# Performance work log

Hardware: AMD Instinct MI355X
Metric: run time of the kernel (lower is better)

## Reference

```python
import jax, jax.numpy as jnp
import numpy as np

DIM = 768
NUM_HEADS = 12
HEAD_DIM = DIM // NUM_HEADS
SCALE = HEAD_DIM ** (-0.5)
WH, WW = 14, 14
NUM_EXTRA = 1
NUM_REL_DIST = (2 * WH - 1) * (2 * WW - 1) + NUM_EXTRA * (NUM_EXTRA + 2)  # 732
N_TOK = WH * WW + NUM_EXTRA  # 197
BATCH = 64


def make_rel_pos_index():
    # mirrors the torch buffer construction (meshgrid 'ij')
    coords = np.stack(np.meshgrid(np.arange(WH), np.arange(WW), indexing='ij'))  # [2,Wh,Ww]
    coords_flat = coords.reshape(2, -1)  # [2, Wh*Ww]
    rel = coords_flat[:, :, None] - coords_flat[:, None, :]  # [2, M, M]
    rel = rel.transpose(1, 2, 0).astype(np.int64)  # [M, M, 2]
    rel[:, :, 0] += WH - 1
    rel[:, :, 1] += WW - 1
    rel[:, :, 0] *= 2 * WW - 1
    idx = np.zeros((N_TOK, N_TOK), dtype=np.int64)
    idx[NUM_EXTRA:, NUM_EXTRA:] = rel.sum(-1)
    idx[0, 0:] = NUM_REL_DIST - 3
    idx[0:, 0] = NUM_REL_DIST - 2
    idx[0, 0] = NUM_REL_DIST - 1
    return jnp.asarray(idx, dtype=jnp.int32)


def setup_inputs() -> dict:
    key = jax.random.key(0)
    ks = jax.random.split(key, 7)
    x = jax.random.normal(ks[0], (BATCH, N_TOK, DIM), dtype=jnp.float32)
    qkv_w = jax.random.normal(ks[1], (3 * DIM, DIM), dtype=jnp.float32) * (DIM ** -0.5)
    q_bias = jax.random.normal(ks[2], (DIM,), dtype=jnp.float32) * 0.02
    v_bias = jax.random.normal(ks[3], (DIM,), dtype=jnp.float32) * 0.02
    rpb_table = jax.random.normal(ks[4], (NUM_REL_DIST, NUM_HEADS), dtype=jnp.float32) * 0.02
    proj_w = jax.random.normal(ks[5], (DIM, DIM), dtype=jnp.float32) * (DIM ** -0.5)
    proj_b = jax.random.normal(ks[6], (DIM,), dtype=jnp.float32) * 0.02
    rel_index = make_rel_pos_index()
    return {"x": x, "qkv_w": qkv_w, "q_bias": q_bias, "v_bias": v_bias,
            "rpb_table": rpb_table, "proj_w": proj_w, "proj_b": proj_b,
            "rel_index": rel_index}


def reference(x, qkv_w, q_bias, v_bias, rpb_table, proj_w, proj_b, rel_index):
    B, N, C = x.shape
    # qkv bias: [q_bias, zeros, v_bias]
    qkv_bias = jnp.concatenate([q_bias, jnp.zeros_like(v_bias), v_bias]).astype(x.dtype)
    qkv = x @ qkv_w.T + qkv_bias  # [B,N,3C]
    qkv = qkv.reshape(B, N, 3, NUM_HEADS, HEAD_DIM).transpose(2, 0, 3, 1, 4)  # [3,B,H,N,d]
    q, k, v = qkv[0] * SCALE, qkv[1], qkv[2]
    # fp32 scores, as in the original
    attn = jnp.einsum('bhnd,bhmd->bhnm', q.astype(jnp.float32), k.astype(jnp.float32))
    # relative position bias gather: [N,N,H] -> [H,N,N]
    bias = rpb_table[rel_index.reshape(-1)].reshape(N, N, NUM_HEADS).transpose(2, 0, 1)
    attn = jax.nn.softmax(attn + bias[None].astype(jnp.float32), axis=-1)
    out = jnp.einsum('bhnm,bhmd->bhnd', attn, v.astype(attn.dtype))
    out = out.transpose(0, 2, 1, 3).reshape(B, N, -1).astype(x.dtype)
    return out @ proj_w.T + proj_b
```

## Files before the change

kernel.cpp:

```cpp
#include <hip/hip_runtime.h>
#include <hip/hip_bf16.h>

#define DIM 768
#define NHEADS 12
#define HD 64
#define NTOK 197
#define BATCH 64
#define NTOKENS (BATCH*NTOK)
#define NPAIR (NTOK*NTOK)
#define QK_SCALE 0.125f
#define CDIM 2304

typedef short bf16x8 __attribute__((ext_vector_type(8)));
typedef float f32x4 __attribute__((ext_vector_type(4)));

#define MFMA(a,b,c) __builtin_amdgcn_mfma_f32_16x16x32_bf16(a,b,c,0,0,0)

__device__ __forceinline__ unsigned short f2bf(float f) {
    union { float f; unsigned u; } v; v.f = f;
    unsigned r = v.u + 0x7FFFu + ((v.u >> 16) & 1u);
    return (unsigned short)(r >> 16);
}

__device__ __forceinline__ float bf2f(unsigned short u) {
    union { unsigned v; float f; } x; x.v = ((unsigned)u) << 16; return x.f;
}

__device__ __forceinline__ void gload16(const unsigned short* g, unsigned short* l) {
    __builtin_amdgcn_global_load_lds(
        (const __attribute__((address_space(1))) void*)g,
        (__attribute__((address_space(3))) void*)l, 16, 0, 0);
}

__device__ __forceinline__ int xcd_swz(int orig, int nwg) {
    int q = nwg >> 3, r = nwg & 7;
    int xcd = orig & 7, idx = orig >> 3;
    return (xcd < r ? xcd * (q + 1) : r * (q + 1) + (xcd - r) * q) + idx;
}

#define NB_X 4728
#define NB_WQ 864
#define NB_WP 288
#define NB_BIAS 1820

__device__ __forceinline__ void cvt8(const float* __restrict__ s,
                                     unsigned short* __restrict__ d, int t, int n8) {
    if (t >= n8) return;
    float4 a = ((const float4*)s)[t * 2], b = ((const float4*)s)[t * 2 + 1];
    union { unsigned short u[8]; bf16x8 v; } p;
    p.u[0] = f2bf(a.x); p.u[1] = f2bf(a.y); p.u[2] = f2bf(a.z); p.u[3] = f2bf(a.w);
    p.u[4] = f2bf(b.x); p.u[5] = f2bf(b.y); p.u[6] = f2bf(b.z); p.u[7] = f2bf(b.w);
    ((bf16x8*)d)[t] = p.v;
}

__global__ __launch_bounds__(256) void prep(
    const float* __restrict__ x, const float* __restrict__ qw,
    const float* __restrict__ pw, const float* __restrict__ rpb,
    const int* __restrict__ rel,
    unsigned short* __restrict__ Xb, unsigned short* __restrict__ Wqb,
    unsigned short* __restrict__ Wpb, unsigned short* __restrict__ biasm)
{
    int bid = blockIdx.x;
    if (bid < NB_X) {
        cvt8(x, Xb, bid * 256 + threadIdx.x, NB_X * 256);
    } else if (bid < NB_X + NB_WQ) {
        cvt8(qw, Wqb, (bid - NB_X) * 256 + threadIdx.x, NB_WQ * 256);
    } else if (bid < NB_X + NB_WQ + NB_WP) {
        cvt8(pw, Wpb, (bid - NB_X - NB_WQ) * 256 + threadIdx.x, NB_WP * 256);
    } else {
        int t = (bid - NB_X - NB_WQ - NB_WP) * 256 + threadIdx.x;
        if (t < NHEADS * NPAIR) {
            int h = t / NPAIR, p = t - h * NPAIR;
            biasm[t] = f2bf(rpb[rel[p] * NHEADS + h]);
        }
    }
}

__global__ __launch_bounds__(256, 2) void gemm_qkv128(
    const unsigned short* __restrict__ Xb, const unsigned short* __restrict__ Wb,
    const float* __restrict__ qbias, const float* __restrict__ vbias,
    unsigned short* __restrict__ QKVb)
{
    __shared__ __attribute__((aligned(16))) unsigned short As[128 * 64];
    __shared__ __attribute__((aligned(16))) unsigned short Bs[128 * 64];
    int tid = threadIdx.x, lane = tid & 63, wid = tid >> 6;
    int wg = xcd_swz(blockIdx.x, 1782);
    int bx = wg / 18, by = wg % 18;
    int m0 = bx * 128, n0 = by * 128;
    int wm = (wid >> 1) * 64, wn = (wid & 1) * 64;

    size_t abase[4], bbase[4];
    unsigned short *alds[4], *blds[4];
    #pragma unroll
    for (int i = 0; i < 4; ++i) {
        int chunk = i * 4 + wid;
        int row = chunk * 8 + (lane >> 3);
        int slot = (lane & 7) ^ (row & 7);
        int ar = m0 + row; if (ar >= NTOKENS) ar = NTOKENS - 1;
        abase[i] = (size_t)ar * DIM + slot * 8;
        bbase[i] = (size_t)(n0 + row) * DIM + slot * 8;
        alds[i] = &As[chunk * 512];
        blds[i] = &Bs[chunk * 512];
    }
    int r15 = lane & 15, hi = lane >> 4, sx = lane & 7;
    int s0 = (hi ^ sx) * 8, s1 = ((hi + 4) ^ sx) * 8;
    int arow[4], brow[4];
    #pragma unroll
    for (int i = 0; i < 4; ++i) {
        arow[i] = (wm + i * 16 + r15) * 64;
        brow[i] = (wn + i * 16 + r15) * 64;
    }

    f32x4 acc[4][4];
    #pragma unroll
    for (int i = 0; i < 4; ++i)
        #pragma unroll
        for (int j = 0; j < 4; ++j) acc[i][j] = (f32x4){0.f, 0.f, 0.f, 0.f};

    for (int k0 = 0; k0 < DIM; k0 += 64) {
        __syncthreads();
        #pragma unroll
        for (int i = 0; i < 4; ++i) {
            gload16(Xb + abase[i] + k0, alds[i]);
            gload16(Wb + bbase[i] + k0, blds[i]);
        }
        __syncthreads();
        #pragma unroll
        for (int ks = 0; ks < 2; ++ks) {
            int so = ks ? s1 : s0;
            bf16x8 af[4], bwv[4];
            #pragma unroll
            for (int i = 0; i < 4; ++i) af[i] = *(bf16x8*)&As[arow[i] + so];
            #pragma unroll
            for (int j = 0; j < 4; ++j) bwv[j] = *(bf16x8*)&Bs[brow[j] + so];
            __builtin_amdgcn_s_setprio(1);
            #pragma unroll
            for (int i = 0; i < 4; ++i)
                #pragma unroll
                for (int j = 0; j < 4; ++j)
                    acc[i][j] = MFMA(af[i], bwv[j], acc[i][j]);
            __builtin_amdgcn_s_setprio(0);
        }
    }
    __syncthreads();

    unsigned short* reg = (wid < 2) ? &As[wid * 4096] : &Bs[(wid - 2) * 4096];
    {
        int which = n0 / DIM;
        float scl = (which == 0) ? QK_SCALE : 1.f;
        #pragma unroll
        for (int j = 0; j < 4; ++j) {
            int colr = n0 - which * DIM + wn + j * 16 + r15;
            float bv = (which == 0) ? qbias[colr] : (which == 2 ? vbias[colr] : 0.f);
            #pragma unroll
            for (int i = 0; i < 4; ++i) {
                #pragma unroll
                for (int r = 0; r < 4; ++r) {
                    int lr = i * 16 + hi * 4 + r;
                    int c = j * 16 + r15;
                    reg[lr * 64 + (c ^ (((lr >> 2) & 3) << 4))] =
                        f2bf((acc[i][j][r] + bv) * scl);
                }
            }
        }
    }
    #pragma unroll
    for (int it = 0; it < 8; ++it) {
        int c = it * 64 + lane;
        int lr = c >> 3, cc = c & 7;
        int row = m0 + wm + lr;
        if (row < NTOKENS) {
            bf16x8 v = *(bf16x8*)&reg[lr * 64 + ((cc * 8) ^ (((lr >> 2) & 3) << 4))];
            *(bf16x8*)(QKVb + (size_t)row * CDIM + n0 + wn + cc * 8) = v;
        }
    }
}

__global__ __launch_bounds__(256, 2) void gemm_proj(
    const unsigned short* __restrict__ Ob, const unsigned short* __restrict__ Wp,
    const float* __restrict__ pbias, float* __restrict__ out)
{
    __shared__ __attribute__((aligned(16))) unsigned short As[128 * 64];
    __shared__ __attribute__((aligned(16))) unsigned short Bs[128 * 64];
    int tid = threadIdx.x, lane = tid & 63, wid = tid >> 6;
    int wg = xcd_swz(blockIdx.x, 594);
    int bx = wg / 6, by = wg % 6;
    int m0 = bx * 128, n0 = by * 128;
    int wm = (wid >> 1) * 64, wn = (wid & 1) * 64;

    size_t abase[4], bbase[4];
    unsigned short *alds[4], *blds[4];
    #pragma unroll
    for (int i = 0; i < 4; ++i) {
        int chunk = i * 4 + wid;
        int row = chunk * 8 + (lane >> 3);
        int slot = (lane & 7) ^ (row & 7);
        int ar = m0 + row; if (ar >= NTOKENS) ar = NTOKENS - 1;
        abase[i] = (size_t)ar * DIM + slot * 8;
        bbase[i] = (size_t)(n0 + row) * DIM + slot * 8;
        alds[i] = &As[chunk * 512];
        blds[i] = &Bs[chunk * 512];
    }
    int r15 = lane & 15, hi = lane >> 4, sx = lane & 7;
    int s0 = (hi ^ sx) * 8, s1 = ((hi + 4) ^ sx) * 8;
    int arow[4], brow[4];
    #pragma unroll
    for (int i = 0; i < 4; ++i) {
        arow[i] = (wm + i * 16 + r15) * 64;
        brow[i] = (wn + i * 16 + r15) * 64;
    }

    f32x4 acc[4][4];
    #pragma unroll
    for (int i = 0; i < 4; ++i)
        #pragma unroll
        for (int j = 0; j < 4; ++j) acc[i][j] = (f32x4){0.f, 0.f, 0.f, 0.f};

    for (int k0 = 0; k0 < DIM; k0 += 64) {
        __syncthreads();
        #pragma unroll
        for (int i = 0; i < 4; ++i) {
            gload16(Ob + abase[i] + k0, alds[i]);
            gload16(Wp + bbase[i] + k0, blds[i]);
        }
        __syncthreads();
        #pragma unroll
        for (int ks = 0; ks < 2; ++ks) {
            int so = ks ? s1 : s0;
            bf16x8 af[4], bwv[4];
            #pragma unroll
            for (int i = 0; i < 4; ++i) af[i] = *(bf16x8*)&As[arow[i] + so];
            #pragma unroll
            for (int j = 0; j < 4; ++j) bwv[j] = *(bf16x8*)&Bs[brow[j] + so];
            __builtin_amdgcn_s_setprio(1);
            #pragma unroll
            for (int i = 0; i < 4; ++i)
                #pragma unroll
                for (int j = 0; j < 4; ++j)
                    acc[i][j] = MFMA(af[i], bwv[j], acc[i][j]);
            __builtin_amdgcn_s_setprio(0);
        }
    }

    #pragma unroll
    for (int j = 0; j < 4; ++j) {
        int col = n0 + wn + j * 16 + r15;
        float bv = pbias[col];
        #pragma unroll
        for (int i = 0; i < 4; ++i) {
            #pragma unroll
            for (int r = 0; r < 4; ++r) {
                int row = m0 + wm + i * 16 + hi * 4 + r;
                if (row < NTOKENS)
                    out[(size_t)row * DIM + col] = acc[i][j][r] + bv;
            }
        }
    }
}

#define KP 72
#define PP 232
#define VPITCH 256

__global__ __launch_bounds__(256, 2) void attn(
    const unsigned short* __restrict__ QKV, const unsigned short* __restrict__ biasm,
    unsigned short* __restrict__ O)
{
    __shared__ __attribute__((aligned(16))) unsigned short VT[64 * VPITCH];
    __shared__ __attribute__((aligned(16))) unsigned short KlPl[208 * KP];

    int tid = threadIdx.x, lane = tid & 63, wid = tid >> 6;
    int r15 = lane & 15, hi = lane >> 4;
    int wg = blockIdx.x;
    int g = wg >> 5, qt = (wg >> 3) & 3, p = wg & 7;
    int bh = g * 8 + p;
    int h = bh % NHEADS, b = bh / NHEADS;
    size_t tb = (size_t)b * NTOK;
    int hq = h * 64;
    int rbase = qt * 64 + wid * 16 + hi * 4;

    int kcol = (tid & 7) * 8;
    bf16x8 kreg[7];
    #pragma unroll
    for (int t = 0; t < 7; ++t) {
        int row = t * 32 + (tid >> 3);
        int rc = row < NTOK ? row : (NTOK - 1);
        kreg[t] = *(const bf16x8*)(QKV + (tb + rc) * CDIM + 768 + hq + kcol);
    }
    #pragma unroll
    for (int t = 0; t < 7; ++t) {
        int row = t * 32 + (tid >> 3);
        if (row < NTOK)
            *(bf16x8*)&KlPl[row * KP + kcol] = kreg[t];
    }

    bf16x8 v0r[4], v1r[4];
    #pragma unroll
    for (int it = 0; it < 4; ++it) {
        int c = it * 256 + tid;
        int rp = c >> 3, kc = c & 7;
        int r0 = 2 * rp, r1 = 2 * rp + 1;
        bf16x8 z = (bf16x8)(short)0;
        v0r[it] = z; v1r[it] = z;
        if (r0 < NTOK) v0r[it] = *(const bf16x8*)(QKV + (tb + r0) * CDIM + 1536 + hq + kc * 8);
        if (r1 < NTOK) v1r[it] = *(const bf16x8*)(QKV + (tb + r1) * CDIM + 1536 + hq + kc * 8);
    }

    int qrow_g = qt * 64 + wid * 16 + r15;
    int qsrc = qrow_g < NTOK ? qrow_g : (NTOK - 1);
    bf16x8 aq[2];
    #pragma unroll
    for (int ks = 0; ks < 2; ++ks)
        aq[ks] = *(const bf16x8*)(QKV + (tb + qsrc) * CDIM + hq + ks * 32 + hi * 8);

    unsigned short breg[4][13];
    {
        const unsigned short* bb = biasm + h * NPAIR;
        #pragma unroll
        for (int r = 0; r < 4; ++r) {
            int row_g = rbase + r;
            int rowc = row_g < NTOK ? row_g : (NTOK - 1);
            const unsigned short* brow = bb + rowc * NTOK + r15;
            #pragma unroll
            for (int t = 0; t < 13; ++t) {
                int off = t * 16;
                if (t == 12 && r15 >= 5) off = 0;
                breg[r][t] = brow[off];
            }
        }
    }
    __syncthreads();

    f32x4 sa[13];
    #pragma unroll
    for (int t = 0; t < 13; ++t) sa[t] = (f32x4){0.f,0.f,0.f,0.f};
    __builtin_amdgcn_s_setprio(1);
    #pragma unroll
    for (int t = 0; t < 13; ++t) {
        #pragma unroll
        for (int ks = 0; ks < 2; ++ks) {
            bf16x8 bk = *(bf16x8*)&KlPl[(t * 16 + r15) * KP + ks * 32 + hi * 8];
            sa[t] = MFMA(aq[ks], bk, sa[t]);
        }
    }
    __builtin_amdgcn_s_setprio(0);
    __syncthreads();

    #pragma unroll
    for (int it = 0; it < 4; ++it) {
        int c = it * 256 + tid;
        int rp = c >> 3, kc = c & 7;
        if (rp < 112) {
            #pragma unroll
            for (int j = 0; j < 8; ++j) {
                unsigned int w = (unsigned int)(unsigned short)v0r[it][j] |
                                 ((unsigned int)(unsigned short)v1r[it][j] << 16);
                int slot2 = (rp >> 2) ^ j ^ kc;
                *(unsigned int*)&VT[(kc * 8 + j) * VPITCH + slot2 * 8 + (rp & 3) * 2] = w;
            }
        }
    }

    int plbase = wid * (16 * PP);
    float invr[4];
    #pragma unroll
    for (int r = 0; r < 4; ++r) {
        #pragma unroll
        for (int t = 0; t < 13; ++t) {
            int col = t * 16 + r15;
            if (col < NTOK) sa[t][r] += bf2f(breg[r][t]);
            else            sa[t][r] = -1e30f;
        }
        float mx = sa[0][r];
        #pragma unroll
        for (int t = 1; t < 13; ++t) mx = fmaxf(mx, sa[t][r]);
        #pragma unroll
        for (int m = 1; m < 16; m <<= 1) mx = fmaxf(mx, __shfl_xor(mx, m));
        float sum = 0.f;
        #pragma unroll
        for (int t = 0; t < 13; ++t) {
            float e = __expf(sa[t][r] - mx);
            sa[t][r] = e; sum += e;
        }
        int roff = plbase + (hi * 4 + r) * PP;
        #pragma unroll
        for (int t = 0; t < 13; ++t)
            KlPl[roff + t * 16 + r15] = f2bf(sa[t][r]);
        KlPl[roff + 208 + r15] = 0;
        #pragma unroll
        for (int m = 1; m < 16; m <<= 1) sum += __shfl_xor(sum, m);
        invr[r] = __builtin_amdgcn_rcpf(sum);
    }
    __syncthreads();

    f32x4 oa[4];
    #pragma unroll
    for (int dt = 0; dt < 4; ++dt) oa[dt] = (f32x4){0.f,0.f,0.f,0.f};
    int X = hi ^ (r15 & 7) ^ (r15 >> 3);
    __builtin_amdgcn_s_setprio(1);
    #pragma unroll
    for (int ks = 0; ks < 7; ++ks) {
        bf16x8 ap = *(bf16x8*)&KlPl[plbase + r15 * PP + ks * 32 + hi * 8];
        #pragma unroll
        for (int dt = 0; dt < 4; ++dt) {
            int d = dt * 16 + r15;
            int slotp = (ks * 4) ^ (dt * 2) ^ X;
            bf16x8 bv = *(bf16x8*)&VT[d * VPITCH + slotp * 8];
            oa[dt] = MFMA(ap, bv, oa[dt]);
        }
    }
    __builtin_amdgcn_s_setprio(0);

    #pragma unroll
    for (int dt = 0; dt < 4; ++dt)
        #pragma unroll
        for (int r = 0; r < 4; ++r)
            KlPl[plbase + (hi * 4 + r) * 72 + dt * 16 + r15] = f2bf(oa[dt][r] * invr[r]);
    #pragma unroll
    for (int it = 0; it < 2; ++it) {
        int c = it * 64 + lane;
        int lr = c >> 3, cc = c & 7;
        int qrow = qt * 64 + wid * 16 + lr;
        if (qrow < NTOK)
            *(bf16x8*)(O + (tb + qrow) * DIM + hq + cc * 8) =
                *(bf16x8*)&KlPl[plbase + lr * 72 + cc * 8];
    }
}

extern "C" void kernel_launch(void* const* d_in, const int* in_sizes, int n_in,
                              void* d_out, int out_size, void* d_ws, size_t ws_size,
                              hipStream_t stream) {
    const float* x      = (const float*)d_in[0];
    const float* qkv_w  = (const float*)d_in[1];
    const float* q_bias = (const float*)d_in[2];
    const float* v_bias = (const float*)d_in[3];
    const float* rpb    = (const float*)d_in[4];
    const float* proj_w = (const float*)d_in[5];
    const float* proj_b = (const float*)d_in[6];
    const int*   rel    = (const int*)d_in[7];
    float* out = (float*)d_out;

    const size_t NELEM = (size_t)NTOKENS * DIM;
    const size_t WQKV  = (size_t)3 * DIM * DIM;
    const size_t WPROJ = (size_t)DIM * DIM;
    unsigned short* Xb   = (unsigned short*)d_ws;
    unsigned short* Wqb  = Xb + NELEM;
    unsigned short* Wpb  = Wqb + WQKV;
    unsigned short* QKVb = Wpb + WPROJ;
    unsigned short* biasm = QKVb + (size_t)NTOKENS * CDIM;
    unsigned short* Ob = Xb;

    prep<<<NB_X + NB_WQ + NB_WP + NB_BIAS, 256, 0, stream>>>(
        x, qkv_w, proj_w, rpb, rel, Xb, Wqb, Wpb, biasm);

    gemm_qkv128<<<1782, 256, 0, stream>>>(Xb, Wqb, q_bias, v_bias, QKVb);

    attn<<<3072, 256, 0, stream>>>(QKVb, biasm, Ob);

    gemm_proj<<<594, 256, 0, stream>>>(Ob, Wpb, proj_b, out);
}
```

Baseline: 155.0 us.

## Enlarge QKV GEMM tile to 256x128 and use packed bf16 conversions in attention

The QKV GEMM moves from 128x128 to 256x128 tiles, with each wave computing 128x64. The grid shrinks from 1782 to 900 blocks and more MFMAs run per K-step, which raises data reuse per LDS load but also raises register pressure and LDS use. In the attention kernel, the scalar f32-to-bf16 rounding uses the hardware v_cvt_pk_bf16_f32 instruction instead, and the V transpose packing uses v_perm_b32, which cuts VALU instruction count. The epilogue is split into two halves so it can reuse the A tile LDS.

```diff
diff --git a/kernel.cpp b/kernel.cpp
--- a/kernel.cpp
+++ b/kernel.cpp
@@ -24,6 +24,18 @@
 
 __device__ __forceinline__ float bf2f(unsigned short u) {
     union { unsigned v; float f; } x; x.v = ((unsigned)u) << 16; return x.f;
+}
+
+__device__ __forceinline__ unsigned cvtpk(float lo, float hi) {
+    unsigned d;
+    asm("v_cvt_pk_bf16_f32 %0, %1, %2" : "=v"(d) : "v"(lo), "v"(hi));
+    return d;
+}
+
+__device__ __forceinline__ unsigned vperm(unsigned s0, unsigned s1, unsigned sel) {
+    unsigned d;
+    asm("v_perm_b32 %0, %1, %2, %3" : "=v"(d) : "v"(s0), "v"(s1), "s"(sel));
+    return d;
 }
 
 __device__ __forceinline__ void gload16(const unsigned short* g, unsigned short* l) {
@@ -76,102 +88,101 @@
     }
 }
 
-__global__ __launch_bounds__(256, 2) void gemm_qkv128(
+__global__ __launch_bounds__(256, 2) void gemm_qkv256(
     const unsigned short* __restrict__ Xb, const unsigned short* __restrict__ Wb,
     const float* __restrict__ qbias, const float* __restrict__ vbias,
     unsigned short* __restrict__ QKVb)
 {
-    __shared__ __attribute__((aligned(16))) unsigned short As[128 * 64];
+    __shared__ __attribute__((aligned(16))) unsigned short As[256 * 64];
     __shared__ __attribute__((aligned(16))) unsigned short Bs[128 * 64];
     int tid = threadIdx.x, lane = tid & 63, wid = tid >> 6;
-    int wg = xcd_swz(blockIdx.x, 1782);
+    int wg = xcd_swz(blockIdx.x, 900);
     int bx = wg / 18, by = wg % 18;
-    int m0 = bx * 128, n0 = by * 128;
-    int wm = (wid >> 1) * 64, wn = (wid & 1) * 64;
-
-    size_t abase[4], bbase[4];
-    unsigned short *alds[4], *blds[4];
+    int m0 = bx * 256, n0 = by * 128;
+    int wm = (wid >> 1) * 128, wn = (wid & 1) * 64;
+    int r15 = lane & 15, hi = lane >> 4, sx = lane & 7;
+    int sl0 = hi ^ sx, sl1 = (hi + 4) ^ sx;
+
+    int slot8 = ((lane & 7) ^ (lane >> 3)) * 8;
+    unsigned asrc[8];
+    #pragma unroll
+    for (int i = 0; i < 8; ++i) {
+        int row = i * 32 + wid * 8 + (lane >> 3);
+        int ar = m0 + row; if (ar >= NTOKENS) ar = NTOKENS - 1;
+        asrc[i] = (unsigned)(ar * DIM + slot8);
+    }
+    unsigned bsrc[4];
     #pragma unroll
     for (int i = 0; i < 4; ++i) {
-        int chunk = i * 4 + wid;
-        int row = chunk * 8 + (lane >> 3);
-        int slot = (lane & 7) ^ (row & 7);
-        int ar = m0 + row; if (ar >= NTOKENS) ar = NTOKENS - 1;
-        abase[i] = (size_t)ar * DIM + slot * 8;
-        bbase[i] = (size_t)(n0 + row) * DIM + slot * 8;
-        alds[i] = &As[chunk * 512];
-        blds[i] = &Bs[chunk * 512];
-    }
-    int r15 = lane & 15, hi = lane >> 4, sx = lane & 7;
-    int s0 = (hi ^ sx) * 8, s1 = ((hi + 4) ^ sx) * 8;
-    int arow[4], brow[4];
-    #pragma unroll
-    for (int i = 0; i < 4; ++i) {
-        arow[i] = (wm + i * 16 + r15) * 64;
-        brow[i] = (wn + i * 16 + r15) * 64;
-    }
-
-    f32x4 acc[4][4];
-    #pragma unroll
-    for (int i = 0; i < 4; ++i)
+        int row = i * 32 + wid * 8 + (lane >> 3);
+        bsrc[i] = (unsigned)((n0 + row) * DIM + slot8);
+    }
+
+    f32x4 acc[8][4];
+    #pragma unroll
+    for (int i = 0; i < 8; ++i)
         #pragma unroll
         for (int j = 0; j < 4; ++j) acc[i][j] = (f32x4){0.f, 0.f, 0.f, 0.f};
 
     for (int k0 = 0; k0 < DIM; k0 += 64) {
         __syncthreads();
         #pragma unroll
-        for (int i = 0; i < 4; ++i) {
-            gload16(Xb + abase[i] + k0, alds[i]);
-            gload16(Wb + bbase[i] + k0, blds[i]);
-        }
+        for (int i = 0; i < 8; ++i)
+            gload16(Xb + asrc[i] + k0, &As[i * 2048 + wid * 512 + lane * 8]);
+        #pragma unroll
+        for (int i = 0; i < 4; ++i)
+            gload16(Wb + bsrc[i] + k0, &Bs[i * 2048 + wid * 512 + lane * 8]);
         __syncthreads();
         #pragma unroll
         for (int ks = 0; ks < 2; ++ks) {
-            int so = ks ? s1 : s0;
-            bf16x8 af[4], bwv[4];
-            #pragma unroll
-            for (int i = 0; i < 4; ++i) af[i] = *(bf16x8*)&As[arow[i] + so];
-            #pragma unroll
-            for (int j = 0; j < 4; ++j) bwv[j] = *(bf16x8*)&Bs[brow[j] + so];
+            int so = (ks ? sl1 : sl0) * 8;
+            bf16x8 af[8], bw[4];
+            #pragma unroll
+            for (int i = 0; i < 8; ++i)
+                af[i] = *(const bf16x8*)&As[(wm + i * 16 + r15) * 64 + so];
+            #pragma unroll
+            for (int j = 0; j < 4; ++j)
+                bw[j] = *(const bf16x8*)&Bs[(wn + j * 16 + r15) * 64 + so];
             __builtin_amdgcn_s_setprio(1);
             #pragma unroll
-            for (int i = 0; i < 4; ++i)
+            for (int i = 0; i < 8; ++i)
                 #pragma unroll
                 for (int j = 0; j < 4; ++j)
-                    acc[i][j] = MFMA(af[i], bwv[j], acc[i][j]);
+                    acc[i][j] = MFMA(af[i], bw[j], acc[i][j]);
             __builtin_amdgcn_s_setprio(0);
         }
     }
     __syncthreads();
 
-    unsigned short* reg = (wid < 2) ? &As[wid * 4096] : &Bs[(wid - 2) * 4096];
-    {
-        int which = n0 / DIM;
-        float scl = (which == 0) ? QK_SCALE : 1.f;
+    unsigned short* reg = &As[wid * 4096];
+    int which = n0 / DIM;
+    float scl = (which == 0) ? QK_SCALE : 1.f;
+    #pragma unroll
+    for (int h = 0; h < 2; ++h) {
         #pragma unroll
         for (int j = 0; j < 4; ++j) {
             int colr = n0 - which * DIM + wn + j * 16 + r15;
             float bv = (which == 0) ? qbias[colr] : (which == 2 ? vbias[colr] : 0.f);
             #pragma unroll
-            for (int i = 0; i < 4; ++i) {
+            for (int mi = 0; mi < 4; ++mi) {
                 #pragma unroll
                 for (int r = 0; r < 4; ++r) {
-                    int lr = i * 16 + hi * 4 + r;
+                    int lr = mi * 16 + hi * 4 + r;
                     int c = j * 16 + r15;
                     reg[lr * 64 + (c ^ (((lr >> 2) & 3) << 4))] =
-                        f2bf((acc[i][j][r] + bv) * scl);
+                        f2bf((acc[h * 4 + mi][j][r] + bv) * scl);
                 }
             }
         }
-    }
-    #pragma unroll
-    for (int it = 0; it < 8; ++it) {
-        int c = it * 64 + lane;
-        int lr = c >> 3, cc = c & 7;
-        int row = m0 + wm + lr;
-        if (row < NTOKENS) {
-            bf16x8 v = *(bf16x8*)&reg[lr * 64 + ((cc * 8) ^ (((lr >> 2) & 3) << 4))];
-            *(bf16x8*)(QKVb + (size_t)row * CDIM + n0 + wn + cc * 8) = v;
+        #pragma unroll
+        for (int it = 0; it < 8; ++it) {
+            int c = it * 64 + lane;
+            int lr = c >> 3, cc = c & 7;
+            int row = m0 + wm + h * 64 + lr;
+            if (row < NTOKENS) {
+                bf16x8 v = *(bf16x8*)&reg[lr * 64 + ((cc * 8) ^ (((lr >> 2) & 3) << 4))];
+                *(bf16x8*)(QKVb + (size_t)row * CDIM + n0 + wn + cc * 8) = v;
+            }
         }
     }
 }
@@ -351,12 +362,17 @@
         int c = it * 256 + tid;
         int rp = c >> 3, kc = c & 7;
         if (rp < 112) {
-            #pragma unroll
-            for (int j = 0; j < 8; ++j) {
-                unsigned int w = (unsigned int)(unsigned short)v0r[it][j] |
-                                 ((unsigned int)(unsigned short)v1r[it][j] << 16);
-                int slot2 = (rp >> 2) ^ j ^ kc;
-                *(unsigned int*)&VT[(kc * 8 + j) * VPITCH + slot2 * 8 + (rp & 3) * 2] = w;
+            union { bf16x8 v; unsigned u[4]; } a0, a1;
+            a0.v = v0r[it]; a1.v = v1r[it];
+            #pragma unroll
+            for (int rr = 0; rr < 4; ++rr) {
+                unsigned we = vperm(a1.u[rr], a0.u[rr], 0x05040100u);
+                unsigned wo = vperm(a1.u[rr], a0.u[rr], 0x07060302u);
+                int j0 = 2 * rr, j1 = 2 * rr + 1;
+                int s20 = (rp >> 2) ^ j0 ^ kc;
+                int s21 = (rp >> 2) ^ j1 ^ kc;
+                *(unsigned*)&VT[(kc * 8 + j0) * VPITCH + s20 * 8 + (rp & 3) * 2] = we;
+                *(unsigned*)&VT[(kc * 8 + j1) * VPITCH + s21 * 8 + (rp & 3) * 2] = wo;
             }
         }
     }
@@ -384,8 +400,12 @@
         }
         int roff = plbase + (hi * 4 + r) * PP;
         #pragma unroll
-        for (int t = 0; t < 13; ++t)
-            KlPl[roff + t * 16 + r15] = f2bf(sa[t][r]);
+        for (int tp = 0; tp < 6; ++tp) {
+            unsigned u = cvtpk(sa[2 * tp][r], sa[2 * tp + 1][r]);
+            KlPl[roff + (2 * tp) * 16 + r15] = (unsigned short)u;
+            KlPl[roff + (2 * tp + 1) * 16 + r15] = (unsigned short)(u >> 16);
+        }
+        KlPl[roff + 192 + r15] = f2bf(sa[12][r]);
         KlPl[roff + 208 + r15] = 0;
         #pragma unroll
         for (int m = 1; m < 16; m <<= 1) sum += __shfl_xor(sum, m);
@@ -412,10 +432,15 @@
     __builtin_amdgcn_s_setprio(0);
 
     #pragma unroll
-    for (int dt = 0; dt < 4; ++dt)
-        #pragma unroll
-        for (int r = 0; r < 4; ++r)
-            KlPl[plbase + (hi * 4 + r) * 72 + dt * 16 + r15] = f2bf(oa[dt][r] * invr[r]);
+    for (int r = 0; r < 4; ++r) {
+        int roff = plbase + (hi * 4 + r) * 72;
+        #pragma unroll
+        for (int dp = 0; dp < 2; ++dp) {
+            unsigned u = cvtpk(oa[2 * dp][r] * invr[r], oa[2 * dp + 1][r] * invr[r]);
+            KlPl[roff + (2 * dp) * 16 + r15] = (unsigned short)u;
+            KlPl[roff + (2 * dp + 1) * 16 + r15] = (unsigned short)(u >> 16);
+        }
+    }
     #pragma unroll
     for (int it = 0; it < 2; ++it) {
         int c = it * 64 + lane;
@@ -453,7 +478,7 @@
     prep<<<NB_X + NB_WQ + NB_WP + NB_BIAS, 256, 0, stream>>>(
         x, qkv_w, proj_w, rpb, rel, Xb, Wqb, Wpb, biasm);
 
-    gemm_qkv128<<<1782, 256, 0, stream>>>(Xb, Wqb, q_bias, v_bias, QKVb);
+    gemm_qkv256<<<900, 256, 0, stream>>>(Xb, Wqb, q_bias, v_bias, QKVb);
 
     attn<<<3072, 256, 0, stream>>>(QKVb, biasm, Ob);
 
```

After: 141.2 us. 1.1x faster.
